# Performance work log

Measured on AMD Instinct MI355X. Metric: run time of the kernel, lower is better.

Reference implementation:

```python
import jax, jax.numpy as jnp
import numpy as np

N_NODES = 20000
N_EDGES = 32000
BN_EPS = 1e-5


def _w(key, fan_in, fan_out):
    return jax.random.normal(key, (fan_in, fan_out), jnp.float32) / np.sqrt(fan_in).astype(np.float32)


def setup_inputs() -> dict:
    key = jax.random.key(0)
    ks = jax.random.split(key, 16)
    x = jax.random.normal(ks[0], (N_NODES, 5120), jnp.float32)
    edge_index = jax.random.randint(ks[1], (2, N_EDGES), 0, N_NODES, dtype=jnp.int64)
    return dict(
        x=x,
        W1l=_w(ks[2], 5120, 1680), b1=jnp.zeros((1680,), jnp.float32), W1r=_w(ks[3], 5120, 1680),
        W2l=_w(ks[4], 1680, 640), b2=jnp.zeros((640,), jnp.float32), W2r=_w(ks[5], 1680, 640),
        bn_gamma=jax.random.uniform(ks[6], (1680,), jnp.float32, 0.5, 1.5),
        bn_beta=jax.random.normal(ks[7], (1680,), jnp.float32) * 0.1,
        bn_mean=jnp.zeros((1680,), jnp.float32),
        bn_var=jnp.ones((1680,), jnp.float32),
        lin1_W=_w(ks[8], 640, 320), lin1_b=jnp.zeros((320,), jnp.float32),
        lin2_W=_w(ks[9], 320, 160), lin2_b=jnp.zeros((160,), jnp.float32),
        lin3_W=_w(ks[10], 160, 2), lin3_b=jnp.zeros((2,), jnp.float32),
        edge_index=edge_index,
    )


def _segment_mean(feat, dst, n):
    # mean-aggregate messages feat[e] into their destination node; 0 for isolated nodes (PyG semantics)
    s = jax.ops.segment_sum(feat, dst, num_segments=n)
    cnt = jax.ops.segment_sum(jnp.ones((dst.shape[0],), feat.dtype), dst, num_segments=n)
    return s / jnp.maximum(cnt, 1.0)[:, None]


def reference(x, W1l, b1, W1r, W2l, b2, W2r, bn_gamma, bn_beta, bn_mean, bn_var,
              lin1_W, lin1_b, lin2_W, lin2_b, lin3_W, lin3_b, edge_index):
    src, dst = edge_index[0], edge_index[1]
    n = x.shape[0]
    # SAGEConv 1: lin_l(mean_j x_j) + lin_r(x_i)
    h = _segment_mean(x[src], dst, n) @ W1l + b1 + x @ W1r
    h = jax.nn.relu(h)
    # BatchNorm1d in eval mode (running stats); dropout inactive in eval
    h = (h - bn_mean) * jax.lax.rsqrt(bn_var + BN_EPS) * bn_gamma + bn_beta
    # SAGEConv 2
    h2 = _segment_mean(h[src], dst, n) @ W2l + b2 + h @ W2r
    o = jax.nn.relu(h2)
    o = jax.nn.relu(o @ lin1_W + lin1_b)
    o = jax.nn.relu(o @ lin2_W + lin2_b)
    return o @ lin3_W + lin3_b
```

## Files before the change

### kernel.cpp

```cpp
#include <hip/hip_runtime.h>
#include <stdint.h>

#define NN 20000
#define NE 32000
#define BN_EPS 1e-5f

typedef __attribute__((ext_vector_type(8))) __bf16 bf16x8;
typedef __attribute__((ext_vector_type(4))) float f32x4;
typedef unsigned short u16;
typedef uint32_t u32;

__device__ __forceinline__ u16 f2bf(float f) {
    u32 u = __float_as_uint(f);
    u += 0x7FFFu + ((u >> 16) & 1u);
    return (u16)(u >> 16);
}
__device__ __forceinline__ float bf2f(u16 u) {
    return __uint_as_float(((u32)u) << 16);
}

__device__ __forceinline__ void gload_lds16(const void* g, void* l) {
    __builtin_amdgcn_global_load_lds(
        (const __attribute__((address_space(1))) void*)g,
        (__attribute__((address_space(3))) void*)(uintptr_t)l,
        16, 0, 0);
}


#define LDSRD(base, r, cb) (*(const bf16x8*)((const char*)(base) + (r)*128 + (cb)))

#define DS_A(apb, qm) do { \
  _Pragma("unroll") for (int m4_ = 0; m4_ < 4; ++m4_) { \
    int r_ = (qm)*128 + m4_*32 + wr16 + lrow; \
    aR[m4_][0] = LDSRD(apb, r_, cb0); \
    aR[m4_][1] = LDSRD(apb, r_, cb1); \
  } } while (0)

#define DS_B(bpb, qn) do { \
  _Pragma("unroll") for (int n2_ = 0; n2_ < 2; ++n2_) { \
    int n_ = (qn)*2 + n2_; \
    int r_ = n_*64 + wc16 + lrow; \
    bR[n_][0] = LDSRD(bpb, r_, cb0); \
    bR[n_][1] = LDSRD(bpb, r_, cb1); \
  } } while (0)

#define MM(qm, qn) do { \
  _Pragma("unroll") for (int m4_ = 0; m4_ < 4; ++m4_) \
  _Pragma("unroll") for (int n2_ = 0; n2_ < 2; ++n2_) { \
    int mi_ = (qm)*4 + m4_, ni_ = (qn)*2 + n2_; \
    acc[mi_][ni_] = __builtin_amdgcn_mfma_f32_16x16x32_bf16(aR[m4_][0], bR[ni_][0], acc[mi_][ni_], 0, 0, 0); \
    acc[mi_][ni_] = __builtin_amdgcn_mfma_f32_16x16x32_bf16(aR[m4_][1], bR[ni_][1], acc[mi_][ni_], 0, 0, 0); \
  } } while (0)

#define STG(Mat, ld, r0, rmax, t, ldsb) do { \
  int ks_ = (t) * 64; if (ks_ > Km64) ks_ = Km64; \
  int ra_ = (r0) + row0;      ra_ = ra_ < (rmax) ? ra_ : (rmax) - 1; \
  int rb_ = (r0) + row0 + 64; rb_ = rb_ < (rmax) ? rb_ : (rmax) - 1; \
  char* d_ = (char*)(ldsb) + dstoff; \
  gload_lds16((Mat) + (size_t)ra_ * (ld) + ks_ + kel, d_); \
  gload_lds16((Mat) + (size_t)rb_ * (ld) + ks_ + kel, d_ + 8192); \
} while (0)

#define SA(b, ha, t) STG(A, lda, m0 + (ha)*128, M, t, &As[b][(ha)*128][0])
#define SB(b, hb, t) STG(B, ldb, n0 + (hb)*128, N, t, &Bs[b][(hb)*128][0])

#define PHASE_TOP() do { __builtin_amdgcn_s_barrier(); \
  asm volatile("s_waitcnt lgkmcnt(0)" ::: "memory"); \
  __builtin_amdgcn_s_setprio(1); } while (0)
#define PHASE_END() do { __builtin_amdgcn_s_setprio(0); \
  __builtin_amdgcn_s_barrier(); } while (0)
#define PHASE_END_VM() do { __builtin_amdgcn_s_setprio(0); \
  asm volatile("s_waitcnt vmcnt(6)" ::: "memory"); \
  __builtin_amdgcn_s_barrier(); } while (0)

__global__ __launch_bounds__(512, 2) void gemm256(
    const u16* __restrict__ A, const u16* __restrict__ B, u16* __restrict__ C,
    int M, int N, int K, int lda, int ldb, int ldc)
{
    __shared__ __align__(16) u16 As[2][256][64];
    __shared__ __align__(16) u16 Bs[2][256][64];

    const int nmt = (M + 255) >> 8;
    const int ntn = (N + 255) >> 8;
    const int nwg = nmt * ntn;

    int bid = blockIdx.x;
    int q8 = nwg >> 3, r8 = nwg & 7;
    int xcd = bid & 7, lid = bid >> 3;
    int wgid = (xcd < r8 ? xcd * (q8 + 1) : r8 * (q8 + 1) + (xcd - r8) * q8) + lid;
    int per = ntn << 3;
    int g = wgid / per;
    int first = g << 3;
    int gsz = nmt - first; gsz = gsz < 8 ? gsz : 8;
    int rem = wgid - g * per;
    int mt = first + rem % gsz;
    int nt = rem / gsz;

    const int m0 = mt << 8, n0 = nt << 8;
    const int tid = threadIdx.x;
    const int wid = tid >> 6, ln = tid & 63;
    const int wr = wid >> 2, wc = wid & 3;
    const int lrow = ln & 15, khi = ln >> 4;
    const int wr16 = wr << 4, wc16 = wc << 4;
    const int cb0 = (khi << 4) ^ ((lrow & 7) << 4);
    const int cb1 = cb0 ^ 64;
    const int row0 = tid >> 3;
    const int kel = ((tid & 7) ^ (row0 & 7)) << 3;
    const int dstoff = (tid & 448) << 4;
    const int Km64 = K - 64;

    f32x4 acc[8][4];
#pragma unroll
    for (int m = 0; m < 8; ++m)
#pragma unroll
        for (int n = 0; n < 4; ++n)
#pragma unroll
            for (int j = 0; j < 4; ++j) acc[m][n][j] = 0.f;
    bf16x8 aR[4][2], bR[4][2];

    SA(0, 0, 0); SB(0, 0, 0); SB(0, 1, 0); SA(0, 1, 0);
    SA(1, 0, 1); SB(1, 0, 1); SB(1, 1, 1);
    asm volatile("s_waitcnt vmcnt(6)" ::: "memory");
    __builtin_amdgcn_s_barrier();

    const int nit = K >> 7;
    for (int it = 0; it < nit; ++it) {
        const int t1 = 2 * it + 1, t2 = 2 * it + 2, t3 = 2 * it + 3;
        DS_A(&As[0][0][0], 0); DS_B(&Bs[0][0][0], 0);
        SA(1, 1, t1);
        PHASE_TOP(); MM(0, 0); PHASE_END();
        DS_B(&Bs[0][0][0], 1);
        SA(0, 0, t2);
        PHASE_TOP(); MM(0, 1); PHASE_END();
        DS_A(&As[0][0][0], 1);
        SB(0, 0, t2);
        PHASE_TOP(); MM(1, 1); PHASE_END();
        SB(0, 1, t2);
        __builtin_amdgcn_s_barrier();
        __builtin_amdgcn_s_setprio(1);
        MM(1, 0);
        PHASE_END_VM();
        DS_A(&As[1][0][0], 0); DS_B(&Bs[1][0][0], 0);
        SA(0, 1, t2);
        PHASE_TOP(); MM(0, 0); PHASE_END();
        DS_B(&Bs[1][0][0], 1);
        SA(1, 0, t3);
        PHASE_TOP(); MM(0, 1); PHASE_END();
        DS_A(&As[1][0][0], 1);
        SB(1, 0, t3);
        PHASE_TOP(); MM(1, 1); PHASE_END();
        SB(1, 1, t3);
        __builtin_amdgcn_s_barrier();
        __builtin_amdgcn_s_setprio(1);
        MM(1, 0);
        PHASE_END_VM();
    }

#pragma unroll
    for (int m = 0; m < 8; ++m) {
        int gr0 = m0 + m * 32 + wr16 + (khi << 2);
#pragma unroll
        for (int n = 0; n < 4; ++n) {
            int gc = n0 + n * 64 + wc16 + lrow;
            if (gc >= N) continue;
#pragma unroll
            for (int j = 0; j < 4; ++j) {
                int gr = gr0 + j;
                if (gr >= M) continue;
                C[(size_t)gr * ldc + gc] = f2bf(acc[m][n][j]);
            }
        }
    }
}

template <int EPI>
__global__ __launch_bounds__(256, 2) void gemm_bt(
    const u16* __restrict__ A, const u16* __restrict__ B, u16* __restrict__ C,
    const float* __restrict__ bias, int M, int N, int K, int lda, int ldb, int ldc)
{
    __shared__ __align__(16) u16 As[128][64];
    __shared__ __align__(16) u16 Bs[128][64];

    const int nmt = (M + 127) >> 7;
    const int ntn = (N + 127) >> 7;
    int bid = blockIdx.x;
    int per_grp = 16 * ntn;
    int g = bid / per_grp;
    int first = g * 16;
    int gsz = min(16, nmt - first);
    int rem = bid - g * per_grp;
    int mt = first + rem % gsz;
    int nt = rem / gsz;

    const int m0 = mt << 7, n0 = nt << 7;
    const int tid = threadIdx.x;
    const int wv = tid >> 6, ln = tid & 63;
    const int wr = wv >> 1, wc = wv & 1;

    f32x4 acc[4][4];
#pragma unroll
    for (int m = 0; m < 4; ++m)
#pragma unroll
        for (int n = 0; n < 4; ++n)
#pragma unroll
            for (int j = 0; j < 4; ++j) acc[m][n][j] = 0.f;

    const int lrow = ln & 15;
    const int koff = (ln >> 4) << 3;

    for (int k0 = 0; k0 < K; k0 += 64) {
#pragma unroll
        for (int r = 0; r < 4; ++r) {
            int c = r * 256 + wv * 64 + ln;
            int row = c >> 3;
            int kc = (c & 7) << 3;
            int ga = m0 + row; ga = ga < M ? ga : M - 1;
            gload_lds16(A + (size_t)ga * lda + (k0 + kc),
                        (char*)&As[0][0] + (size_t)(r * 256 + wv * 64) * 16);
            int gb = n0 + row; gb = gb < N ? gb : N - 1;
            gload_lds16(B + (size_t)gb * ldb + (k0 + kc),
                        (char*)&Bs[0][0] + (size_t)(r * 256 + wv * 64) * 16);
        }
        __syncthreads();
#pragma unroll
        for (int kk = 0; kk < 2; ++kk) {
            bf16x8 af[4], bfr[4];
            const int krd = (kk << 5) + koff;
#pragma unroll
            for (int m = 0; m < 4; ++m)
                af[m] = *(const bf16x8*)&As[(wr << 6) + (m << 4) + lrow][krd];
#pragma unroll
            for (int n = 0; n < 4; ++n)
                bfr[n] = *(const bf16x8*)&Bs[(wc << 6) + (n << 4) + lrow][krd];
#pragma unroll
            for (int m = 0; m < 4; ++m)
#pragma unroll
                for (int n = 0; n < 4; ++n)
                    acc[m][n] = __builtin_amdgcn_mfma_f32_16x16x32_bf16(
                        af[m], bfr[n], acc[m][n], 0, 0, 0);
        }
        __syncthreads();
    }

    const int colb = ln & 15;
    const int rowb = (ln >> 4) << 2;
#pragma unroll
    for (int m = 0; m < 4; ++m) {
        int gr0 = m0 + (wr << 6) + (m << 4) + rowb;
#pragma unroll
        for (int n = 0; n < 4; ++n) {
            int gc = n0 + (wc << 6) + (n << 4) + colb;
            if (gc >= N) continue;
            float bv = (EPI == 1) ? bias[gc] : 0.f;
#pragma unroll
            for (int j = 0; j < 4; ++j) {
                int gr = gr0 + j;
                if (gr >= M) continue;
                float v = acc[m][n][j];
                if (EPI == 1) { v += bv; v = v > 0.f ? v : 0.f; }
                C[(size_t)gr * ldc + gc] = f2bf(v);
            }
        }
    }
}

__global__ void cvt_bf16(const float* __restrict__ in, u16* __restrict__ out, int n4)
{
    for (int i = blockIdx.x * 256 + threadIdx.x; i < n4; i += gridDim.x * 256) {
        float4 v = ((const float4*)in)[i];
        ushort4 o;
        o.x = f2bf(v.x); o.y = f2bf(v.y); o.z = f2bf(v.z); o.w = f2bf(v.w);
        ((ushort4*)out)[i] = o;
    }
}

__global__ void wtrans(const float* __restrict__ s0, const float* __restrict__ s1,
                       u16* __restrict__ out, int Kin, int Kpad, int N, int nsplit)
{
    __shared__ float t[32][33];
    int k0 = blockIdx.x << 5, n0 = blockIdx.y << 5;
    int tx = threadIdx.x, ty = threadIdx.y;
#pragma unroll
    for (int i = 0; i < 4; ++i) {
        int k = k0 + ty + (i << 3);
        int n = n0 + tx;
        float v = 0.f;
        if (k < Kin && n < N)
            v = (n < nsplit) ? s0[(size_t)k * nsplit + n]
                             : s1[(size_t)k * (N - nsplit) + (n - nsplit)];
        t[ty + (i << 3)][tx] = v;
    }
    __syncthreads();
#pragma unroll
    for (int i = 0; i < 4; ++i) {
        int n = n0 + ty + (i << 3);
        int k = k0 + tx;
        if (n < N && k < Kpad)
            out[(size_t)n * Kpad + k] = f2bf(t[tx][ty + (i << 3)]);
    }
}

__global__ void deg_k(const int* __restrict__ dst, int* __restrict__ deg, int ne)
{
    int e = blockIdx.x * 256 + threadIdx.x;
    if (e < ne) atomicAdd(&deg[dst[e]], 1);
}

__global__ __launch_bounds__(256) void scan_k(const int* __restrict__ deg,
                                              int* __restrict__ off, int* __restrict__ cur)
{
    __shared__ int part[256];
    int t = threadIdx.x;
    int st = t * 79;
    int s = 0;
    for (int j = 0; j < 79; ++j) {
        int idx = st + j;
        if (idx < NN) s += deg[idx];
    }
    part[t] = s;
    __syncthreads();
    for (int d = 1; d < 256; d <<= 1) {
        int v = (t >= d) ? part[t - d] : 0;
        __syncthreads();
        part[t] += v;
        __syncthreads();
    }
    int run = part[t] - s;
    for (int j = 0; j < 79; ++j) {
        int idx = st + j;
        if (idx < NN) {
            off[idx] = run;
            cur[idx] = run;
            run += deg[idx];
        }
    }
    if (t == 255) off[NN] = NE;
}

__global__ void fill_k(const int* __restrict__ src, const int* __restrict__ dst,
                       int* __restrict__ cur, int* __restrict__ esrc, int ne)
{
    int e = blockIdx.x * 256 + threadIdx.x;
    if (e < ne) {
        int p = atomicAdd(&cur[dst[e]], 1);
        esrc[p] = src[e];
    }
}

__device__ __forceinline__ void bn_emit(
    int b, int c, float sx, float sy, float sz, float sw, float inv,
    const u16* __restrict__ y1, const float* __restrict__ b1,
    const float* __restrict__ gam, const float* __restrict__ bet,
    const float* __restrict__ mn, const float* __restrict__ vr, u16* __restrict__ h)
{
    int col = c << 2;
    ushort4 yr = *(const ushort4*)&y1[(size_t)b * 3360 + 1680 + col];
    float4 bb = *(const float4*)&b1[col];
    float4 g4 = *(const float4*)&gam[col];
    float4 be = *(const float4*)&bet[col];
    float4 m4 = *(const float4*)&mn[col];
    float4 v4 = *(const float4*)&vr[col];
    float t0 = fmaxf(sx * inv + bb.x + bf2f(yr.x), 0.f);
    float t1 = fmaxf(sy * inv + bb.y + bf2f(yr.y), 0.f);
    float t2 = fmaxf(sz * inv + bb.z + bf2f(yr.z), 0.f);
    float t3 = fmaxf(sw * inv + bb.w + bf2f(yr.w), 0.f);
    t0 = (t0 - m4.x) * rsqrtf(v4.x + BN_EPS) * g4.x + be.x;
    t1 = (t1 - m4.y) * rsqrtf(v4.y + BN_EPS) * g4.y + be.y;
    t2 = (t2 - m4.z) * rsqrtf(v4.z + BN_EPS) * g4.z + be.z;
    t3 = (t3 - m4.w) * rsqrtf(v4.w + BN_EPS) * g4.w + be.w;
    ushort4 o;
    o.x = f2bf(t0); o.y = f2bf(t1); o.z = f2bf(t2); o.w = f2bf(t3);
    *(ushort4*)&h[(size_t)b * 1792 + col] = o;
}

__global__ __launch_bounds__(256) void agg_bn_k(
    const u16* __restrict__ y1, const int* __restrict__ off, const int* __restrict__ esrc,
    const float* __restrict__ b1, const float* __restrict__ gam, const float* __restrict__ bet,
    const float* __restrict__ mn, const float* __restrict__ vr, u16* __restrict__ h)
{
    int b = blockIdx.x, t = threadIdx.x;
    int o0 = off[b], o1 = off[b + 1];
    int deg = o1 - o0;
    const int c0 = t, c1 = t + 256;
    float s0x = 0.f, s0y = 0.f, s0z = 0.f, s0w = 0.f;
    float s1x = 0.f, s1y = 0.f, s1z = 0.f, s1w = 0.f;
    for (int j = o0; j < o1; ++j) {
        int s = esrc[j];
        const u16* row = y1 + (size_t)s * 3360;
        ushort4 v = *(const ushort4*)&row[c0 << 2];
        s0x += bf2f(v.x); s0y += bf2f(v.y); s0z += bf2f(v.z); s0w += bf2f(v.w);
        if (t < 164) {
            ushort4 w = *(const ushort4*)&row[c1 << 2];
            s1x += bf2f(w.x); s1y += bf2f(w.y); s1z += bf2f(w.z); s1w += bf2f(w.w);
        }
    }
    float inv = 1.f / (deg > 1 ? (float)deg : 1.f);
    bn_emit(b, c0, s0x, s0y, s0z, s0w, inv, y1, b1, gam, bet, mn, vr, h);
    if (t < 164) {
        bn_emit(b, c1, s1x, s1y, s1z, s1w, inv, y1, b1, gam, bet, mn, vr, h);
    } else if (t < 192) {
        ushort4 z; z.x = 0; z.y = 0; z.z = 0; z.w = 0;
        *(ushort4*)&h[(size_t)b * 1792 + (c1 << 2)] = z;
    }
}

__global__ __launch_bounds__(192) void agg_h2_k(
    const u16* __restrict__ y2, const int* __restrict__ off, const int* __restrict__ esrc,
    const float* __restrict__ b2, u16* __restrict__ h2)
{
    int b = blockIdx.x, t = threadIdx.x;
    if (t >= 160) return;
    int o0 = off[b], o1 = off[b + 1];
    int deg = o1 - o0;
    float sx = 0.f, sy = 0.f, sz = 0.f, sw = 0.f;
    for (int j = o0; j < o1; ++j) {
        int s = esrc[j];
        ushort4 v = *(const ushort4*)&y2[(size_t)s * 1280 + (t << 2)];
        sx += bf2f(v.x); sy += bf2f(v.y); sz += bf2f(v.z); sw += bf2f(v.w);
    }
    float inv = 1.f / (deg > 1 ? (float)deg : 1.f);
    int col = t << 2;
    ushort4 yr = *(const ushort4*)&y2[(size_t)b * 1280 + 640 + col];
    float4 bb = *(const float4*)&b2[col];
    ushort4 o;
    o.x = f2bf(fmaxf(sx * inv + bb.x + bf2f(yr.x), 0.f));
    o.y = f2bf(fmaxf(sy * inv + bb.y + bf2f(yr.y), 0.f));
    o.z = f2bf(fmaxf(sz * inv + bb.z + bf2f(yr.z), 0.f));
    o.w = f2bf(fmaxf(sw * inv + bb.w + bf2f(yr.w), 0.f));
    *(ushort4*)&h2[(size_t)b * 640 + col] = o;
}

__global__ void lin3_k(const u16* __restrict__ o2, const float* __restrict__ W,
                       const float* __restrict__ b, float* __restrict__ out)
{
    __shared__ float ws[320];
    for (int j = threadIdx.x; j < 320; j += 256) ws[j] = W[j];
    __syncthreads();
    int i = blockIdx.x * 256 + threadIdx.x;
    if (i >= NN) return;
    float a0 = b[0], a1 = b[1];
    const u16* row = o2 + (size_t)i * 160;
#pragma unroll
    for (int k8 = 0; k8 < 20; ++k8) {
        ushort4 v0 = *(const ushort4*)&row[k8 * 8];
        ushort4 v1 = *(const ushort4*)&row[k8 * 8 + 4];
        int kb = k8 * 8;
        float f;
        f = bf2f(v0.x); a0 += f * ws[(kb + 0) * 2]; a1 += f * ws[(kb + 0) * 2 + 1];
        f = bf2f(v0.y); a0 += f * ws[(kb + 1) * 2]; a1 += f * ws[(kb + 1) * 2 + 1];
        f = bf2f(v0.z); a0 += f * ws[(kb + 2) * 2]; a1 += f * ws[(kb + 2) * 2 + 1];
        f = bf2f(v0.w); a0 += f * ws[(kb + 3) * 2]; a1 += f * ws[(kb + 3) * 2 + 1];
        f = bf2f(v1.x); a0 += f * ws[(kb + 4) * 2]; a1 += f * ws[(kb + 4) * 2 + 1];
        f = bf2f(v1.y); a0 += f * ws[(kb + 5) * 2]; a1 += f * ws[(kb + 5) * 2 + 1];
        f = bf2f(v1.z); a0 += f * ws[(kb + 6) * 2]; a1 += f * ws[(kb + 6) * 2 + 1];
        f = bf2f(v1.w); a0 += f * ws[(kb + 7) * 2]; a1 += f * ws[(kb + 7) * 2 + 1];
    }
    out[(size_t)i * 2 + 0] = a0;
    out[(size_t)i * 2 + 1] = a1;
}

extern "C" void kernel_launch(void* const* d_in, const int* in_sizes, int n_in,
                              void* d_out, int out_size, void* d_ws, size_t ws_size,
                              hipStream_t stream)
{
    const float* x     = (const float*)d_in[0];
    const float* W1l   = (const float*)d_in[1];
    const float* b1    = (const float*)d_in[2];
    const float* W1r   = (const float*)d_in[3];
    const float* W2l   = (const float*)d_in[4];
    const float* b2    = (const float*)d_in[5];
    const float* W2r   = (const float*)d_in[6];
    const float* gam   = (const float*)d_in[7];
    const float* bet   = (const float*)d_in[8];
    const float* bmean = (const float*)d_in[9];
    const float* bvar  = (const float*)d_in[10];
    const float* l1W   = (const float*)d_in[11];
    const float* l1b   = (const float*)d_in[12];
    const float* l2W   = (const float*)d_in[13];
    const float* l2b   = (const float*)d_in[14];
    const float* l3W   = (const float*)d_in[15];
    const float* l3b   = (const float*)d_in[16];
    const int*   ei    = (const int*)d_in[17];
    const int* src = ei, * dst = ei + NE;

    char* ws = (char*)d_ws;
    u16*   y1   = (u16*)(ws + 0);
    u16*   y2   = (u16*)(ws + 0);
    u16*   o1   = (u16*)(ws + 0);
    u16*   o2   = (u16*)(ws + 16000000);
    u16*   xbf  = (u16*)(ws + 136000000);
    u16*   hbuf = (u16*)(ws + 136000000);
    u16*   h2   = (u16*)(ws + 136000000);
    u16*   w1T  = (u16*)(ws + 341000000);
    u16*   w2T  = (u16*)(ws + 341000000);
    u16*   l1T  = (u16*)(ws + 346000000);
    u16*   l2T  = (u16*)(ws + 347000000);
    int*   deg  = (int*)(ws + 350000000);
    int*   off  = (int*)(ws + 350100000);
    int*   cur  = (int*)(ws + 350200000);
    int*   esrc = (int*)(ws + 350300000);

    cvt_bf16<<<2048, 256, 0, stream>>>(x, xbf, NN * 5120 / 4);
    wtrans<<<dim3(160, 105), dim3(32, 8), 0, stream>>>(W1l, W1r, w1T, 5120, 5120, 3360, 1680);

    gemm256<<<79 * 14, 512, 0, stream>>>(xbf, w1T, y1, NN, 3360, 5120, 5120, 5120, 3360);

    hipMemsetAsync(deg, 0, NN * sizeof(int), stream);
    deg_k<<<(NE + 255) / 256, 256, 0, stream>>>(dst, deg, NE);
    scan_k<<<1, 256, 0, stream>>>(deg, off, cur);
    fill_k<<<(NE + 255) / 256, 256, 0, stream>>>(src, dst, cur, esrc, NE);

    agg_bn_k<<<NN, 256, 0, stream>>>(y1, off, esrc, b1, gam, bet, bmean, bvar, hbuf);

    wtrans<<<dim3(56, 40), dim3(32, 8), 0, stream>>>(W2l, W2r, w2T, 1680, 1792, 1280, 640);

    gemm256<<<79 * 5, 512, 0, stream>>>(hbuf, w2T, y2, NN, 1280, 1792, 1792, 1792, 1280);

    agg_h2_k<<<NN, 192, 0, stream>>>(y2, off, esrc, b2, h2);

    wtrans<<<dim3(20, 10), dim3(32, 8), 0, stream>>>(l1W, l1W, l1T, 640, 640, 320, 320);
    wtrans<<<dim3(10, 5), dim3(32, 8), 0, stream>>>(l2W, l2W, l2T, 320, 320, 160, 160);

    gemm_bt<1><<<157 * 3, 256, 0, stream>>>(h2, l1T, o1, l1b,
                                            NN, 320, 640, 640, 640, 320);

    gemm_bt<1><<<157 * 2, 256, 0, stream>>>(o1, l2T, o2, l2b,
                                            NN, 160, 320, 320, 320, 160);

    lin3_k<<<(NN + 255) / 256, 256, 0, stream>>>(o2, l3W, l3b, (float*)d_out);
}
```

Baseline: 1.102 ms.

## Compute layer-1 neighbor projection only for rows that appear as edge sources

Builds a compacted list of the distinct source nodes before the first GEMM. The x@W1l half is then computed only for those rows, gathered through the list, while x@W1r still covers every node; both run in one launch with work split by role. This cuts the W1l GEMM work to roughly the fraction of nodes that are sources, in exchange for index indirection in the A loads, an extra scan pass, and a lookup remap in the second aggregation.

After: 1.160 ms. 5.2% more time.

```diff
diff --git a/kernel.cpp b/kernel.cpp
--- a/kernel.cpp
+++ b/kernel.cpp
@@ -25,7 +25,6 @@
         (__attribute__((address_space(3))) void*)(uintptr_t)l,
         16, 0, 0);
 }
-
 
 #define LDSRD(base, r, cb) (*(const bf16x8*)((const char*)(base) + (r)*128 + (cb)))
 
@@ -51,18 +50,6 @@
     acc[mi_][ni_] = __builtin_amdgcn_mfma_f32_16x16x32_bf16(aR[m4_][0], bR[ni_][0], acc[mi_][ni_], 0, 0, 0); \
     acc[mi_][ni_] = __builtin_amdgcn_mfma_f32_16x16x32_bf16(aR[m4_][1], bR[ni_][1], acc[mi_][ni_], 0, 0, 0); \
   } } while (0)
-
-#define STG(Mat, ld, r0, rmax, t, ldsb) do { \
-  int ks_ = (t) * 64; if (ks_ > Km64) ks_ = Km64; \
-  int ra_ = (r0) + row0;      ra_ = ra_ < (rmax) ? ra_ : (rmax) - 1; \
-  int rb_ = (r0) + row0 + 64; rb_ = rb_ < (rmax) ? rb_ : (rmax) - 1; \
-  char* d_ = (char*)(ldsb) + dstoff; \
-  gload_lds16((Mat) + (size_t)ra_ * (ld) + ks_ + kel, d_); \
-  gload_lds16((Mat) + (size_t)rb_ * (ld) + ks_ + kel, d_ + 8192); \
-} while (0)
-
-#define SA(b, ha, t) STG(A, lda, m0 + (ha)*128, M, t, &As[b][(ha)*128][0])
-#define SB(b, hb, t) STG(B, ldb, n0 + (hb)*128, N, t, &Bs[b][(hb)*128][0])
 
 #define PHASE_TOP() do { __builtin_amdgcn_s_barrier(); \
   asm volatile("s_waitcnt lgkmcnt(0)" ::: "memory"); \
@@ -72,6 +59,148 @@
 #define PHASE_END_VM() do { __builtin_amdgcn_s_setprio(0); \
   asm volatile("s_waitcnt vmcnt(6)" ::: "memory"); \
   __builtin_amdgcn_s_barrier(); } while (0)
+
+#define KLOOP_BODY(nit_) do { \
+  for (int it = 0; it < (nit_); ++it) { \
+    const int t1 = 2 * it + 1, t2 = 2 * it + 2, t3 = 2 * it + 3; \
+    DS_A(&As[0][0][0], 0); DS_B(&Bs[0][0][0], 0); \
+    SA(1, 1, t1); \
+    PHASE_TOP(); MM(0, 0); PHASE_END(); \
+    DS_B(&Bs[0][0][0], 1); \
+    SA(0, 0, t2); \
+    PHASE_TOP(); MM(0, 1); PHASE_END(); \
+    DS_A(&As[0][0][0], 1); \
+    SB(0, 0, t2); \
+    PHASE_TOP(); MM(1, 1); PHASE_END(); \
+    SB(0, 1, t2); \
+    __builtin_amdgcn_s_barrier(); \
+    __builtin_amdgcn_s_setprio(1); \
+    MM(1, 0); \
+    PHASE_END_VM(); \
+    DS_A(&As[1][0][0], 0); DS_B(&Bs[1][0][0], 0); \
+    SA(0, 1, t2); \
+    PHASE_TOP(); MM(0, 0); PHASE_END(); \
+    DS_B(&Bs[1][0][0], 1); \
+    SA(1, 0, t3); \
+    PHASE_TOP(); MM(0, 1); PHASE_END(); \
+    DS_A(&As[1][0][0], 1); \
+    SB(1, 0, t3); \
+    PHASE_TOP(); MM(1, 1); PHASE_END(); \
+    SB(1, 1, t3); \
+    __builtin_amdgcn_s_barrier(); \
+    __builtin_amdgcn_s_setprio(1); \
+    MM(1, 0); \
+    PHASE_END_VM(); \
+  } } while (0)
+
+__global__ __launch_bounds__(512, 2) void gemm1f(
+    const u16* __restrict__ xbf, const u16* __restrict__ w1T,
+    u16* __restrict__ y1l, u16* __restrict__ y1r,
+    const int* __restrict__ clist, const int* __restrict__ nsrcp)
+{
+    __shared__ __align__(16) u16 As[2][256][64];
+    __shared__ __align__(16) u16 Bs[2][256][64];
+    const int K = 5120, lda = 5120;
+    const int Km64 = K - 64;
+
+    const int nsrc = nsrcp[0];
+    const int nmt_l = (nsrc + 255) >> 8;
+    const int nl = nmt_l * 7;
+
+    int bid = blockIdx.x;
+    const int nwg = 1106;
+    int q8 = nwg >> 3, r8 = nwg & 7;
+    int xcd = bid & 7, lid = bid >> 3;
+    int wgid = (xcd < r8 ? xcd * (q8 + 1) : r8 * (q8 + 1) + (xcd - r8) * q8) + lid;
+
+    int roleL = (wgid < nl);
+    int local, nmt;
+    if (roleL) { local = wgid; nmt = nmt_l; }
+    else {
+        local = wgid - nl;
+        if (local >= 553) return;
+        nmt = 79;
+    }
+    int g = local / 56;
+    int first = g << 3;
+    int gsz = nmt - first; gsz = gsz < 8 ? gsz : 8;
+    int rem = local - g * 56;
+    int mt = first + rem % gsz;
+    int nt = rem / gsz;
+
+    const int m0 = mt << 8, n0 = nt << 8;
+    const int tid = threadIdx.x;
+    const int wid = tid >> 6, ln = tid & 63;
+    const int wr = wid >> 2, wc = wid & 3;
+    const int lrow = ln & 15, khi = ln >> 4;
+    const int wr16 = wr << 4, wc16 = wc << 4;
+    const int cb0 = (khi << 4) ^ ((lrow & 7) << 4);
+    const int cb1 = cb0 ^ 64;
+    const int row0 = tid >> 3;
+    const int kel = ((tid & 7) ^ (row0 & 7)) << 3;
+    const int dstoff = (tid & 448) << 4;
+
+    const u16* Bp = w1T + (roleL ? (size_t)0 : (size_t)1680 * 5120);
+    const u16* aB[4];
+    const u16* bB[4];
+#pragma unroll
+    for (int i = 0; i < 4; ++i) {
+        int r = m0 + ((i >> 1) << 7) + ((i & 1) << 6) + row0;
+        int ga;
+        if (roleL) { int idx = r < nsrc ? r : nsrc - 1; ga = clist[idx]; }
+        else       { ga = r < NN ? r : NN - 1; }
+        aB[i] = xbf + (size_t)ga * lda + kel;
+        int rb = n0 + ((i >> 1) << 7) + ((i & 1) << 6) + row0;
+        rb = rb < 1680 ? rb : 1679;
+        bB[i] = Bp + (size_t)rb * lda + kel;
+    }
+
+#define SA(b, ha, t) do { int ks_ = (t) * 64; if (ks_ > Km64) ks_ = Km64; \
+  char* d_ = (char*)&As[b][(ha)*128][0] + dstoff; \
+  gload_lds16(aB[(ha)*2] + ks_, d_); \
+  gload_lds16(aB[(ha)*2 + 1] + ks_, d_ + 8192); } while (0)
+#define SB(b, hb, t) do { int ks_ = (t) * 64; if (ks_ > Km64) ks_ = Km64; \
+  char* d_ = (char*)&Bs[b][(hb)*128][0] + dstoff; \
+  gload_lds16(bB[(hb)*2] + ks_, d_); \
+  gload_lds16(bB[(hb)*2 + 1] + ks_, d_ + 8192); } while (0)
+
+    f32x4 acc[8][4];
+#pragma unroll
+    for (int m = 0; m < 8; ++m)
+#pragma unroll
+        for (int n = 0; n < 4; ++n)
+#pragma unroll
+            for (int j = 0; j < 4; ++j) acc[m][n][j] = 0.f;
+    bf16x8 aR[4][2], bR[4][2];
+
+    SA(0, 0, 0); SB(0, 0, 0); SB(0, 1, 0); SA(0, 1, 0);
+    SA(1, 0, 1); SB(1, 0, 1); SB(1, 1, 1);
+    asm volatile("s_waitcnt vmcnt(6)" ::: "memory");
+    __builtin_amdgcn_s_barrier();
+
+    KLOOP_BODY(40);
+
+#undef SA
+#undef SB
+
+    const int Meff = roleL ? nsrc : NN;
+    u16* C = roleL ? y1l : y1r;
+#pragma unroll
+    for (int m = 0; m < 8; ++m) {
+        int gr0 = m0 + m * 32 + wr16 + (khi << 2);
+#pragma unroll
+        for (int n = 0; n < 4; ++n) {
+            int gc = n0 + n * 64 + wc16 + lrow;
+            if (gc >= 1680) continue;
+#pragma unroll
+            for (int j = 0; j < 4; ++j) {
+                int gr = gr0 + j;
+                if (gr >= Meff) continue;
+                C[(size_t)gr * 1680 + gc] = f2bf(acc[m][n][j]);
+            }
+        }
+    }
+}
 
 __global__ __launch_bounds__(512, 2) void gemm256(
     const u16* __restrict__ A, const u16* __restrict__ B, u16* __restrict__ C,
@@ -109,6 +238,19 @@
     const int dstoff = (tid & 448) << 4;
     const int Km64 = K - 64;
 
+#define SA(b, ha, t) do { int ks_ = (t) * 64; if (ks_ > Km64) ks_ = Km64; \
+  int ra_ = m0 + (ha)*128 + row0;      ra_ = ra_ < M ? ra_ : M - 1; \
+  int rb_ = m0 + (ha)*128 + row0 + 64; rb_ = rb_ < M ? rb_ : M - 1; \
+  char* d_ = (char*)&As[b][(ha)*128][0] + dstoff; \
+  gload_lds16(A + (size_t)ra_ * lda + ks_ + kel, d_); \
+  gload_lds16(A + (size_t)rb_ * lda + ks_ + kel, d_ + 8192); } while (0)
+#define SB(b, hb, t) do { int ks_ = (t) * 64; if (ks_ > Km64) ks_ = Km64; \
+  int ra_ = n0 + (hb)*128 + row0;      ra_ = ra_ < N ? ra_ : N - 1; \
+  int rb_ = n0 + (hb)*128 + row0 + 64; rb_ = rb_ < N ? rb_ : N - 1; \
+  char* d_ = (char*)&Bs[b][(hb)*128][0] + dstoff; \
+  gload_lds16(B + (size_t)ra_ * ldb + ks_ + kel, d_); \
+  gload_lds16(B + (size_t)rb_ * ldb + ks_ + kel, d_ + 8192); } while (0)
+
     f32x4 acc[8][4];
 #pragma unroll
     for (int m = 0; m < 8; ++m)
@@ -124,37 +266,10 @@
     __builtin_amdgcn_s_barrier();
 
     const int nit = K >> 7;
-    for (int it = 0; it < nit; ++it) {
-        const int t1 = 2 * it + 1, t2 = 2 * it + 2, t3 = 2 * it + 3;
-        DS_A(&As[0][0][0], 0); DS_B(&Bs[0][0][0], 0);
-        SA(1, 1, t1);
-        PHASE_TOP(); MM(0, 0); PHASE_END();
-        DS_B(&Bs[0][0][0], 1);
-        SA(0, 0, t2);
-        PHASE_TOP(); MM(0, 1); PHASE_END();
-        DS_A(&As[0][0][0], 1);
-        SB(0, 0, t2);
-        PHASE_TOP(); MM(1, 1); PHASE_END();
-        SB(0, 1, t2);
-        __builtin_amdgcn_s_barrier();
-        __builtin_amdgcn_s_setprio(1);
-        MM(1, 0);
-        PHASE_END_VM();
-        DS_A(&As[1][0][0], 0); DS_B(&Bs[1][0][0], 0);
-        SA(0, 1, t2);
-        PHASE_TOP(); MM(0, 0); PHASE_END();
-        DS_B(&Bs[1][0][0], 1);
-        SA(1, 0, t3);
-        PHASE_TOP(); MM(0, 1); PHASE_END();
-        DS_A(&As[1][0][0], 1);
-        SB(1, 0, t3);
-        PHASE_TOP(); MM(1, 1); PHASE_END();
-        SB(1, 1, t3);
-        __builtin_amdgcn_s_barrier();
-        __builtin_amdgcn_s_setprio(1);
-        MM(1, 0);
-        PHASE_END_VM();
-    }
+    KLOOP_BODY(nit);
+
+#undef SA
+#undef SB
 
 #pragma unroll
     for (int m = 0; m < 8; ++m) {
@@ -300,61 +415,78 @@
     }
 }
 
-__global__ void deg_k(const int* __restrict__ dst, int* __restrict__ deg, int ne)
+__global__ void deg_mark_k(const int* __restrict__ src, const int* __restrict__ dst,
+                           int* __restrict__ deg, int* __restrict__ cmark, int ne)
 {
     int e = blockIdx.x * 256 + threadIdx.x;
-    if (e < ne) atomicAdd(&deg[dst[e]], 1);
-}
-
-__global__ __launch_bounds__(256) void scan_k(const int* __restrict__ deg,
-                                              int* __restrict__ off, int* __restrict__ cur)
+    if (e < ne) {
+        atomicAdd(&deg[dst[e]], 1);
+        cmark[src[e]] = 1;
+    }
+}
+
+__global__ __launch_bounds__(256) void scan2_k(
+    const int* __restrict__ deg, int* __restrict__ off, int* __restrict__ cur,
+    int* __restrict__ cmark, int* __restrict__ clist, int* __restrict__ nsrcp)
 {
     __shared__ int part[256];
     int t = threadIdx.x;
     int st = t * 79;
     int s = 0;
-    for (int j = 0; j < 79; ++j) {
-        int idx = st + j;
-        if (idx < NN) s += deg[idx];
-    }
+    for (int j = 0; j < 79; ++j) { int i = st + j; if (i < NN) s += deg[i]; }
     part[t] = s;
     __syncthreads();
     for (int d = 1; d < 256; d <<= 1) {
         int v = (t >= d) ? part[t - d] : 0;
-        __syncthreads();
-        part[t] += v;
-        __syncthreads();
+        __syncthreads(); part[t] += v; __syncthreads();
     }
     int run = part[t] - s;
     for (int j = 0; j < 79; ++j) {
-        int idx = st + j;
-        if (idx < NN) {
-            off[idx] = run;
-            cur[idx] = run;
-            run += deg[idx];
+        int i = st + j;
+        if (i < NN) { off[i] = run; cur[i] = run; run += deg[i]; }
+    }
+    if (t == 255) off[NN] = NE;
+    __syncthreads();
+    int s2 = 0;
+    for (int j = 0; j < 79; ++j) { int i = st + j; if (i < NN) s2 += cmark[i]; }
+    part[t] = s2;
+    __syncthreads();
+    for (int d = 1; d < 256; d <<= 1) {
+        int v = (t >= d) ? part[t - d] : 0;
+        __syncthreads(); part[t] += v; __syncthreads();
+    }
+    int run2 = part[t] - s2;
+    for (int j = 0; j < 79; ++j) {
+        int i = st + j;
+        if (i < NN) {
+            int m = cmark[i];
+            if (m) clist[run2] = i;
+            cmark[i] = run2;
+            run2 += m;
         }
     }
-    if (t == 255) off[NN] = NE;
+    if (t == 255) nsrcp[0] = part[255];
 }
 
 __global__ void fill_k(const int* __restrict__ src, const int* __restrict__ dst,
-                       int* __restrict__ cur, int* __restrict__ esrc, int ne)
+                       int* __restrict__ cur, const int* __restrict__ cidx,
+                       int* __restrict__ esrc, int ne)
 {
     int e = blockIdx.x * 256 + threadIdx.x;
     if (e < ne) {
         int p = atomicAdd(&cur[dst[e]], 1);
-        esrc[p] = src[e];
+        esrc[p] = cidx[src[e]];
     }
 }
 
 __device__ __forceinline__ void bn_emit(
     int b, int c, float sx, float sy, float sz, float sw, float inv,
-    const u16* __restrict__ y1, const float* __restrict__ b1,
+    const u16* __restrict__ y1r, const float* __restrict__ b1,
     const float* __restrict__ gam, const float* __restrict__ bet,
     const float* __restrict__ mn, const float* __restrict__ vr, u16* __restrict__ h)
 {
     int col = c << 2;
-    ushort4 yr = *(const ushort4*)&y1[(size_t)b * 3360 + 1680 + col];
+    ushort4 yr = *(const ushort4*)&y1r[(size_t)b * 1680 + col];
     float4 bb = *(const float4*)&b1[col];
     float4 g4 = *(const float4*)&gam[col];
     float4 be = *(const float4*)&bet[col];
@@ -374,7 +506,8 @@
 }
 
 __global__ __launch_bounds__(256) void agg_bn_k(
-    const u16* __restrict__ y1, const int* __restrict__ off, const int* __restrict__ esrc,
+    const u16* __restrict__ y1l, const u16* __restrict__ y1r,
+    const int* __restrict__ off, const int* __restrict__ esrc,
     const float* __restrict__ b1, const float* __restrict__ gam, const float* __restrict__ bet,
     const float* __restrict__ mn, const float* __restrict__ vr, u16* __restrict__ h)
 {
@@ -386,7 +519,7 @@
     float s1x = 0.f, s1y = 0.f, s1z = 0.f, s1w = 0.f;
     for (int j = o0; j < o1; ++j) {
         int s = esrc[j];
-        const u16* row = y1 + (size_t)s * 3360;
+        const u16* row = y1l + (size_t)s * 1680;
         ushort4 v = *(const ushort4*)&row[c0 << 2];
         s0x += bf2f(v.x); s0y += bf2f(v.y); s0z += bf2f(v.z); s0w += bf2f(v.w);
         if (t < 164) {
@@ -395,9 +528,9 @@
         }
     }
     float inv = 1.f / (deg > 1 ? (float)deg : 1.f);
-    bn_emit(b, c0, s0x, s0y, s0z, s0w, inv, y1, b1, gam, bet, mn, vr, h);
+    bn_emit(b, c0, s0x, s0y, s0z, s0w, inv, y1r, b1, gam, bet, mn, vr, h);
     if (t < 164) {
-        bn_emit(b, c1, s1x, s1y, s1z, s1w, inv, y1, b1, gam, bet, mn, vr, h);
+        bn_emit(b, c1, s1x, s1y, s1z, s1w, inv, y1r, b1, gam, bet, mn, vr, h);
     } else if (t < 192) {
         ushort4 z; z.x = 0; z.y = 0; z.z = 0; z.w = 0;
         *(ushort4*)&h[(size_t)b * 1792 + (c1 << 2)] = z;
@@ -406,6 +539,7 @@
 
 __global__ __launch_bounds__(192) void agg_h2_k(
     const u16* __restrict__ y2, const int* __restrict__ off, const int* __restrict__ esrc,
+    const int* __restrict__ clist, const int* __restrict__ nsrcp,
     const float* __restrict__ b2, u16* __restrict__ h2)
 {
     int b = blockIdx.x, t = threadIdx.x;
@@ -414,7 +548,7 @@
     int deg = o1 - o0;
     float sx = 0.f, sy = 0.f, sz = 0.f, sw = 0.f;
     for (int j = o0; j < o1; ++j) {
-        int s = esrc[j];
+        int s = clist[esrc[j]];
         ushort4 v = *(const ushort4*)&y2[(size_t)s * 1280 + (t << 2)];
         sx += bf2f(v.x); sy += bf2f(v.y); sz += bf2f(v.z); sw += bf2f(v.w);
     }
@@ -484,7 +618,8 @@
     const int* src = ei, * dst = ei + NE;
 
     char* ws = (char*)d_ws;
-    u16*   y1   = (u16*)(ws + 0);
+    u16*   y1l  = (u16*)(ws + 0);
+    u16*   y1r  = (u16*)(ws + 68000000);
     u16*   y2   = (u16*)(ws + 0);
     u16*   o1   = (u16*)(ws + 0);
     u16*   o2   = (u16*)(ws + 16000000);
@@ -495,28 +630,32 @@
     u16*   w2T  = (u16*)(ws + 341000000);
     u16*   l1T  = (u16*)(ws + 346000000);
     u16*   l2T  = (u16*)(ws + 347000000);
-    int*   deg  = (int*)(ws + 350000000);
-    int*   off  = (int*)(ws + 350100000);
-    int*   cur  = (int*)(ws + 350200000);
-    int*   esrc = (int*)(ws + 350300000);
+    int*   deg   = (int*)(ws + 375500000);
+    int*   off   = (int*)(ws + 375584000);
+    int*   cur   = (int*)(ws + 375668000);
+    int*   cmark = (int*)(ws + 375752000);
+    int*   clist = (int*)(ws + 375836000);
+    int*   esrc  = (int*)(ws + 375920000);
+    int*   nsrcp = (int*)(ws + 376050000);
+
+    hipMemsetAsync(deg, 0, NN * sizeof(int), stream);
+    hipMemsetAsync(cmark, 0, NN * sizeof(int), stream);
+    deg_mark_k<<<(NE + 255) / 256, 256, 0, stream>>>(src, dst, deg, cmark, NE);
+    scan2_k<<<1, 256, 0, stream>>>(deg, off, cur, cmark, clist, nsrcp);
+    fill_k<<<(NE + 255) / 256, 256, 0, stream>>>(src, dst, cur, cmark, esrc, NE);
 
     cvt_bf16<<<2048, 256, 0, stream>>>(x, xbf, NN * 5120 / 4);
     wtrans<<<dim3(160, 105), dim3(32, 8), 0, stream>>>(W1l, W1r, w1T, 5120, 5120, 3360, 1680);
 
-    gemm256<<<79 * 14, 512, 0, stream>>>(xbf, w1T, y1, NN, 3360, 5120, 5120, 5120, 3360);
-
-    hipMemsetAsync(deg, 0, NN * sizeof(int), stream);
-    deg_k<<<(NE + 255) / 256, 256, 0, stream>>>(dst, deg, NE);
-    scan_k<<<1, 256, 0, stream>>>(deg, off, cur);
-    fill_k<<<(NE + 255) / 256, 256, 0, stream>>>(src, dst, cur, esrc, NE);
-
-    agg_bn_k<<<NN, 256, 0, stream>>>(y1, off, esrc, b1, gam, bet, bmean, bvar, hbuf);
+    gemm1f<<<1106, 512, 0, stream>>>(xbf, w1T, y1l, y1r, clist, nsrcp);
+
+    agg_bn_k<<<NN, 256, 0, stream>>>(y1l, y1r, off, esrc, b1, gam, bet, bmean, bvar, hbuf);
 
     wtrans<<<dim3(56, 40), dim3(32, 8), 0, stream>>>(W2l, W2r, w2T, 1680, 1792, 1280, 640);
 
     gemm256<<<79 * 5, 512, 0, stream>>>(hbuf, w2T, y2, NN, 1280, 1792, 1792, 1792, 1280);
 
-    agg_h2_k<<<NN, 192, 0, stream>>>(y2, off, esrc, b2, h2);
+    agg_h2_k<<<NN, 192, 0, stream>>>(y2, off, esrc, clist, nsrcp, b2, h2);
 
     wtrans<<<dim3(20, 10), dim3(32, 8), 0, stream>>>(l1W, l1W, l1T, 640, 640, 320, 320);
     wtrans<<<dim3(10, 5), dim3(32, 8), 0, stream>>>(l2W, l2W, l2T, 320, 320, 160, 160);
```
